# Kernel optimization log

Measured on AMD Instinct MI355X. Metric: run time of the kernel, lower is better.

The kernel has to match this reference:

```python
import jax, jax.numpy as jnp
import numpy as np

GROUPS = 4  # init kwarg


def setup_inputs() -> dict:
    key = jax.random.key(0)
    k1, k2, k3, k4 = jax.random.split(key, 4)
    B, S, D, H = 4, 4096, 256, 10
    # 0.02 scale on weights keeps unscaled QK^T logits in a sane range
    # (original torch code uses raw randn weights and applies NO 1/sqrt(d)
    # scaling inside group_attention, which saturates softmax).
    return {
        "x": jax.random.normal(k1, (B, S, D), dtype=jnp.float32),
        "Wq": jax.random.normal(k2, (H, D, D), dtype=jnp.float32) * 0.02,
        "Wk": jax.random.normal(k3, (H, D, D), dtype=jnp.float32) * 0.02,
        "Wo": jax.random.normal(k4, (D, H * D), dtype=jnp.float32) * 0.02,
    }


def reference(x, Wq, Wk, Wo):
    # x: [B,S,D]; Wq/Wk: [H,D,D]; Wo: [D, H*D] (nn.Linear weight layout)
    H, D, _ = Wq.shape
    B, S, _ = x.shape
    G = GROUPS
    C = S // G  # chunk length

    Q = jnp.einsum('bsd,hde->hbse', x, Wq)  # [H,B,S,D]
    K = jnp.einsum('bsd,hde->hbse', x, Wk)
    # Faithful to source bug: V is projected with wk weights -> V == K

    Qg = Q.reshape(H, B, G, C, D)
    KVg = jnp.roll(K.reshape(H, B, G, C, D), shift=-1, axis=2)  # chunk i attends chunk (i+1)%G

    # NOTE: original applies NO scaling to logits (scale arg unused)
    S_ = jnp.einsum('hbgqd,hbgkd->hbgqk', Qg, KVg)   # [H,B,G,C,C]
    P = jax.nn.softmax(S_, axis=-1)
    O = jnp.einsum('hbgqk,hbgkd->hbgqd', P, KVg)     # [H,B,G,C,D]

    # concat heads on feature dim: [B,S,H*D]
    out = O.reshape(H, B, S, D).transpose(1, 2, 0, 3).reshape(B, S, H * D)
    return jnp.einsum('bsk,dk->bsd', out, Wo)  # final Linear (no bias)
```

## Files before the change

kernel.cpp:

```cpp
#include <hip/hip_runtime.h>

typedef float f32x4 __attribute__((ext_vector_type(4)));
typedef float f32x16 __attribute__((ext_vector_type(16)));
typedef short s16x8 __attribute__((ext_vector_type(8)));
typedef unsigned int u32;

#define BSZ 4
#define SEQ 4096
#define DIM 256
#define NH 10
#define NG 4
#define CHK 1024
#define BS_TOT 16384
#define HD 2560
#define LOG2E 1.44269504f

__device__ __forceinline__ unsigned short f2bf(float f) {
    unsigned int u = __builtin_bit_cast(unsigned int, f);
    u = (u + 0x7fffu + ((u >> 16) & 1u)) >> 16;
    return (unsigned short)u;
}

__device__ __forceinline__ void gload_lds16(const unsigned short* g, unsigned short* l) {
    __builtin_amdgcn_global_load_lds((const __attribute__((address_space(1))) u32*)g,
                                     (__attribute__((address_space(3))) u32*)l, 16, 0, 0);
}

__device__ __forceinline__ u32 cvtpk_bf16(float lo, float hi) {
    u32 r;
    asm("v_cvt_pk_bf16_f32 %0, %1, %2" : "=v"(r) : "v"(lo), "v"(hi));
    return r;
}



__global__ __launch_bounds__(256) void cast_f32_bf16(const float* __restrict__ s,
                                                     unsigned short* __restrict__ d, int n) {
    long i = 4L * (blockIdx.x * 256 + threadIdx.x);
    if (i < n) {
        float4 v = *(const float4*)(s + i);
        ushort4 o;
        o.x = f2bf(v.x); o.y = f2bf(v.y); o.z = f2bf(v.z); o.w = f2bf(v.w);
        *(ushort4*)(d + i) = o;
    }
}

__global__ __launch_bounds__(256) void transpose_cast_w(const float* __restrict__ Wq,
                                                        const float* __restrict__ Wk,
                                                        unsigned short* __restrict__ wqt,
                                                        unsigned short* __restrict__ wkt) {
    const float* W = (blockIdx.z & 1) ? Wk : Wq;
    unsigned short* Wt = (blockIdx.z & 1) ? wkt : wqt;
    int h = blockIdx.z >> 1;
    __shared__ float tile[32][33];
    int d0 = blockIdx.x * 32, e0 = blockIdx.y * 32;
    int tx = threadIdx.x & 31, ty = threadIdx.x >> 5;
    const float* Wh = W + (long)h * 65536;
    unsigned short* Wth = Wt + (long)h * 65536;
#pragma unroll
    for (int r = ty; r < 32; r += 8) tile[r][tx] = Wh[(long)(d0 + r) * 256 + e0 + tx];
    __syncthreads();
#pragma unroll
    for (int r = ty; r < 32; r += 8) Wth[(long)(e0 + r) * 256 + d0 + tx] = f2bf(tile[tx][r]);
}


__device__ __forceinline__ void gemm_body(const unsigned short* __restrict__ A, long lda,
                                          const unsigned short* __restrict__ Bt, long ldb,
                                          unsigned short* Cb, float* Cf, long ldc,
                                          int K, bool accum, long mbase,
                                          unsigned short* KQo, unsigned short* KTo,
                                          float cscale) {
    __shared__ unsigned short As[64 * 40];
    __shared__ unsigned short Bs[256 * 40];
    const int t = threadIdx.x;
    const int w = t >> 6, l = t & 63, lr = l & 15, lg = l >> 4;

    f32x4 acc[16];
#pragma unroll
    for (int i = 0; i < 16; i++) acc[i] = (f32x4){0.f, 0.f, 0.f, 0.f};

    const int ar = t >> 2, akc = (t & 3) * 8;

    for (int k0 = 0; k0 < K; k0 += 32) {
        *(s16x8*)(&As[ar * 40 + akc]) = *(const s16x8*)(A + (mbase + ar) * lda + k0 + akc);
#pragma unroll
        for (int s = 0; s < 4; s++) {
            int n = s * 64 + (t >> 2);
            *(s16x8*)(&Bs[n * 40 + akc]) = *(const s16x8*)(Bt + (long)n * ldb + k0 + akc);
        }
        __syncthreads();
        s16x8 af = *(const s16x8*)(&As[(w * 16 + lr) * 40 + lg * 8]);
        __builtin_amdgcn_s_setprio(1);
#pragma unroll
        for (int nt = 0; nt < 16; nt++) {
            s16x8 bf = *(const s16x8*)(&Bs[(nt * 16 + lr) * 40 + lg * 8]);
            acc[nt] = __builtin_amdgcn_mfma_f32_16x16x32_bf16(af, bf, acc[nt], 0, 0, 0);
        }
        __builtin_amdgcn_s_setprio(0);
        __syncthreads();
    }
    long m0 = mbase + w * 16 + lg * 4;
    if (Cb || Cf) {
#pragma unroll
        for (int nt = 0; nt < 16; nt++) {
            int col = nt * 16 + lr;
#pragma unroll
            for (int r = 0; r < 4; r++) {
                long idx = (m0 + r) * ldc + col;
                if (Cb) {
                    Cb[idx] = f2bf(acc[nt][r] * cscale);
                } else {
                    float v = acc[nt][r];
                    if (accum) v += Cf[idx];
                    Cf[idx] = v;
                }
            }
        }
    }
    if (KQo) {
        int bg = (int)(m0 >> 10);
        int kin = (int)(m0 & 1023);
        int kt = kin >> 5, kw = kin & 31;
        unsigned short* tb = KQo + (long)bg * (256 * 1024) + (long)kt * 8192;
#pragma unroll
        for (int nt = 0; nt < 16; nt++) {
            int d = nt * 16 + lr;
            unsigned short* p = tb + (d >> 4) * 512 + ((d >> 3) & 1) * 256 + (d & 7);
#pragma unroll
            for (int r = 0; r < 4; r++) p[(kw + r) * 8] = f2bf(acc[nt][r]);
        }
    }
    if (KTo) {
        int bg = (int)(m0 >> 10);
        int key0 = (int)(m0 & 1023);
        int kt = key0 >> 5, kw = key0 & 31;
        unsigned short* base = KTo + (long)bg * (256 * 1024) + (long)kt * 8192
                             + (kw >> 4) * 512 + ((kw >> 3) & 1) * 256 + (kw & 7);
#pragma unroll
        for (int nt = 0; nt < 16; nt++) {
            int col = nt * 16 + lr;
            ushort4 v;
            v.x = f2bf(acc[nt][0]); v.y = f2bf(acc[nt][1]);
            v.z = f2bf(acc[nt][2]); v.w = f2bf(acc[nt][3]);
            *(ushort4*)(base + (col >> 5) * 1024 + (col & 31) * 8) = v;
        }
    }
}

__global__ __launch_bounds__(256) void proj_kernel(const unsigned short* __restrict__ xb,
                                                   const unsigned short* __restrict__ wqt,
                                                   const unsigned short* __restrict__ wkt,
                                                   unsigned short* Qb, unsigned short* KQb,
                                                   unsigned short* KTb,
                                                   int h0, long headStrideOut, long headStrideKT) {
    int h = h0 + blockIdx.y;
    bool isK = (blockIdx.z != 0);
    const unsigned short* Bt = (isK ? wkt : wqt) + (long)h * 65536;
    unsigned short* C = isK ? nullptr : (Qb + (long)blockIdx.y * headStrideOut);
    unsigned short* KQo = isK ? (KQb + (long)blockIdx.y * headStrideKT) : nullptr;
    unsigned short* KTo = isK ? (KTb + (long)blockIdx.y * headStrideKT) : nullptr;
    gemm_body(xb, 256, Bt, 256, C, nullptr, 256, 256, false, (long)blockIdx.x * 64,
              KQo, KTo, isK ? 1.0f : LOG2E);
}

__global__ __launch_bounds__(256) void final_kernel(const unsigned short* __restrict__ Ob, long lda,
                                                    const unsigned short* __restrict__ wob, long ldb,
                                                    float* out, int K, int accum) {
    gemm_body(Ob, lda, wob, ldb, nullptr, out, 256, K, accum != 0, (long)blockIdx.x * 64,
              nullptr, nullptr, 1.0f);
}


__global__ __launch_bounds__(256, 3) void proj128(const unsigned short* __restrict__ xb,
                                                  const unsigned short* __restrict__ wqt,
                                                  const unsigned short* __restrict__ wkt,
                                                  unsigned short* __restrict__ Qb,
                                                  unsigned short* __restrict__ KQb,
                                                  unsigned short* __restrict__ KTb,
                                                  long headStrideOut, long headStrideKT) {
    __shared__ unsigned short As[2][128 * 32];
    __shared__ unsigned short Bs[2][128 * 32];

    const int lb = blockIdx.x;
    const int logical = (lb & 7) * 640 + (lb >> 3);
    const int x = logical / 40;
    const int u = logical - x * 40;
    const int mat = u >> 1, ntile = u & 1;
    const int h = mat >> 1;
    const bool isK = (mat & 1) != 0;

    const unsigned short* A = xb;
    const unsigned short* Bt = (isK ? wkt : wqt) + (long)h * 65536 + (long)ntile * 128 * 256;
    const long mbase = (long)x * 128;
    const int ncol0 = ntile * 128;

    const int t = threadIdx.x, w = t >> 6, l = t & 63, lr = l & 15, lg = l >> 4;
    const int wm = w >> 1, wn = w & 1;

    int sOff[2];
#pragma unroll
    for (int i = 0; i < 2; i++) {
        int row = w * 32 + i * 16 + (l >> 2);
        int cs2 = (l & 3) ^ (row & 3);
        sOff[i] = row * 256 + cs2 * 8;
    }

    f32x4 acc[4][4];
#pragma unroll
    for (int i = 0; i < 4; i++)
#pragma unroll
        for (int j = 0; j < 4; j++) acc[i][j] = (f32x4){0.f, 0.f, 0.f, 0.f};

#define PSTAGE(buf, k0) do {                                                     \
        _Pragma("unroll")                                                        \
        for (int i = 0; i < 2; i++)                                              \
            gload_lds16(A + mbase * 256 + (k0) + sOff[i],                        \
                        &As[buf][(w * 32 + i * 16) * 32]);                       \
        _Pragma("unroll")                                                        \
        for (int i = 0; i < 2; i++)                                              \
            gload_lds16(Bt + (k0) + sOff[i],                                     \
                        &Bs[buf][(w * 32 + i * 16) * 32]);                       \
    } while (0)

    PSTAGE(0, 0);
    __syncthreads();
    int cur = 0;
    for (int ks = 0; ks < 8; ++ks) {
        if (ks < 7) PSTAGE(cur ^ 1, (ks + 1) * 32);
        s16x8 a[4], b[4];
#pragma unroll
        for (int mf = 0; mf < 4; mf++) {
            int row = wm * 64 + mf * 16 + lr;
            a[mf] = *(const s16x8*)(&As[cur][row * 32 + (lg ^ (row & 3)) * 8]);
        }
#pragma unroll
        for (int nf = 0; nf < 4; nf++) {
            int row = wn * 64 + nf * 16 + lr;
            b[nf] = *(const s16x8*)(&Bs[cur][row * 32 + (lg ^ (row & 3)) * 8]);
        }
        __builtin_amdgcn_s_setprio(1);
#pragma unroll
        for (int mf = 0; mf < 4; mf++)
#pragma unroll
            for (int nf = 0; nf < 4; nf++)
                acc[mf][nf] = __builtin_amdgcn_mfma_f32_16x16x32_bf16(a[mf], b[nf], acc[mf][nf], 0, 0, 0);
        __builtin_amdgcn_s_setprio(0);
        __syncthreads();
        cur ^= 1;
    }
#undef PSTAGE

    long m0 = mbase + wm * 64 + lg * 4;
    if (!isK) {
        unsigned short* C = Qb + (long)h * headStrideOut;
#pragma unroll
        for (int mf = 0; mf < 4; mf++) {
            long mrow = m0 + mf * 16;
#pragma unroll
            for (int nf = 0; nf < 4; nf++) {
                int col = ncol0 + wn * 64 + nf * 16 + lr;
#pragma unroll
                for (int r = 0; r < 4; r++)
                    C[(mrow + r) * 256 + col] = f2bf(acc[mf][nf][r] * LOG2E);
            }
        }
    } else {
        unsigned short* KQo = KQb + (long)h * headStrideKT;
        unsigned short* KTo = KTb + (long)h * headStrideKT;
#pragma unroll
        for (int mf = 0; mf < 4; mf++) {
            long key = m0 + mf * 16;
            int bg = (int)(key >> 10), kin = (int)(key & 1023);
            int kt = kin >> 5, kw = kin & 31;
            unsigned short* qtb = KQo + (long)bg * (256 * 1024) + (long)kt * 8192;
            unsigned short* vtb = KTo + (long)bg * (256 * 1024) + (long)kt * 8192
                                + (kw >> 4) * 512 + ((kw >> 3) & 1) * 256 + (kw & 7);
#pragma unroll
            for (int nf = 0; nf < 4; nf++) {
                int d = ncol0 + wn * 64 + nf * 16 + lr;
                unsigned short* p = qtb + (d >> 4) * 512 + ((d >> 3) & 1) * 256 + (d & 7);
#pragma unroll
                for (int r = 0; r < 4; r++) p[(kw + r) * 8] = f2bf(acc[mf][nf][r]);
                ushort4 v;
                v.x = f2bf(acc[mf][nf][0]); v.y = f2bf(acc[mf][nf][1]);
                v.z = f2bf(acc[mf][nf][2]); v.w = f2bf(acc[mf][nf][3]);
                *(ushort4*)(vtb + (d >> 5) * 1024 + (d & 31) * 8) = v;
            }
        }
    }
}


__global__ __launch_bounds__(256, 3) void final128(const unsigned short* __restrict__ Ob,
                                                   long headStride,
                                                   const unsigned short* __restrict__ wob,
                                                   float* __restrict__ out) {
    __shared__ unsigned short As[2][128 * 32];
    __shared__ unsigned short Bs[2][128 * 32];

    const int lb = blockIdx.x;
    const int logical = (lb & 7) * 32 + (lb >> 3);
    const int x = logical >> 1, ntile = logical & 1;
    const long mbase = (long)x * 128;
    const int ncol0 = ntile * 128;
    const unsigned short* Bt = wob + (long)ncol0 * HD;

    const int t = threadIdx.x, w = t >> 6, l = t & 63, lr = l & 15, lg = l >> 4;
    const int wm = w >> 1, wn = w & 1;

    int sOffA[2], sOffB[2];
#pragma unroll
    for (int i = 0; i < 2; i++) {
        int row = w * 32 + i * 16 + (l >> 2);
        int cs2 = (l & 3) ^ (row & 3);
        sOffA[i] = row * 256 + cs2 * 8;
        sOffB[i] = row * HD + cs2 * 8;
    }

    f32x4 acc[4][4];
#pragma unroll
    for (int i = 0; i < 4; i++)
#pragma unroll
        for (int j = 0; j < 4; j++) acc[i][j] = (f32x4){0.f, 0.f, 0.f, 0.f};

#define FSTAGE(buf, k0) do {                                                     \
        const unsigned short* Asrc = Ob + (long)((k0) >> 8) * headStride         \
                                   + mbase * 256 + ((k0) & 255);                 \
        _Pragma("unroll")                                                        \
        for (int i = 0; i < 2; i++)                                              \
            gload_lds16(Asrc + sOffA[i], &As[buf][(w * 32 + i * 16) * 32]);      \
        _Pragma("unroll")                                                        \
        for (int i = 0; i < 2; i++)                                              \
            gload_lds16(Bt + (k0) + sOffB[i], &Bs[buf][(w * 32 + i * 16) * 32]); \
    } while (0)

    FSTAGE(0, 0);
    __syncthreads();
    int cur = 0;
    for (int ks = 0; ks < 80; ++ks) {
        if (ks < 79) FSTAGE(cur ^ 1, (ks + 1) * 32);
        s16x8 a[4], b[4];
#pragma unroll
        for (int mf = 0; mf < 4; mf++) {
            int row = wm * 64 + mf * 16 + lr;
            a[mf] = *(const s16x8*)(&As[cur][row * 32 + (lg ^ (row & 3)) * 8]);
        }
#pragma unroll
        for (int nf = 0; nf < 4; nf++) {
            int row = wn * 64 + nf * 16 + lr;
            b[nf] = *(const s16x8*)(&Bs[cur][row * 32 + (lg ^ (row & 3)) * 8]);
        }
        __builtin_amdgcn_s_setprio(1);
#pragma unroll
        for (int mf = 0; mf < 4; mf++)
#pragma unroll
            for (int nf = 0; nf < 4; nf++)
                acc[mf][nf] = __builtin_amdgcn_mfma_f32_16x16x32_bf16(a[mf], b[nf], acc[mf][nf], 0, 0, 0);
        __builtin_amdgcn_s_setprio(0);
        __syncthreads();
        cur ^= 1;
    }
#undef FSTAGE

    long m0 = mbase + wm * 64 + lg * 4;
#pragma unroll
    for (int mf = 0; mf < 4; mf++) {
        long mrow = m0 + mf * 16;
#pragma unroll
        for (int nf = 0; nf < 4; nf++) {
            int col = ncol0 + wn * 64 + nf * 16 + lr;
#pragma unroll
            for (int r = 0; r < 4; r++) out[(mrow + r) * 256 + col] = acc[mf][nf][r];
        }
    }
}


__global__ __launch_bounds__(256, 2) void attn_kernel(const unsigned short* __restrict__ Qb,
                                                      const unsigned short* __restrict__ KQg,
                                                      long headStrideQK,
                                                      const unsigned short* __restrict__ KTg,
                                                      long headStrideKT,
                                                      unsigned short* __restrict__ Ob,
                                                      long ldo, long colStride,
                                                      int chunkPerXcd) {
    const int lb = blockIdx.x;
    const int logical = (lb & 7) * chunkPerXcd + (lb >> 3);
    const int bx = logical & 7;
    const int by = (logical >> 3) & 15;
    const int h = logical >> 7;

    const unsigned short* Q = Qb + (long)h * colStride;
    const unsigned short* KQ = KQg + (long)h * headStrideQK;
    const unsigned short* KT = KTg + (long)h * headStrideKT;
    unsigned short* O = Ob + (long)h * colStride;
    const int b = by >> 2, g = by & 3;
    const long qrow0 = (long)b * SEQ + (long)g * CHK + (long)bx * 128;
    const int bgk = b * NG + ((g + 1) & 3);
    const unsigned short* KQc = KQ + (long)bgk * (256 * 1024);
    const unsigned short* KTc = KT + (long)bgk * (256 * 1024);

    __shared__ unsigned short Klds[2][8192];
    __shared__ unsigned short Vlds[2][8192];

    const int t = threadIdx.x;
    const int w = t >> 6, l = t & 63, l31 = l & 31, hi = l >> 5;

    s16x8 qf[16];
    {
        const unsigned short* qp = Q + (qrow0 + w * 32 + l31) * 256 + hi * 8;
#pragma unroll
        for (int s = 0; s < 16; s++) qf[s] = *(const s16x8*)(qp + s * 16);
    }

    f32x16 o[8];
#pragma unroll
    for (int i = 0; i < 8; i++)
#pragma unroll
        for (int j = 0; j < 16; j++) o[i][j] = 0.f;
    float l_part = 0.f;

#define STAGE(buf, kt_) do {                                                    \
        const unsigned short* Ks = KQc + (long)(kt_) * 8192 + l * 8;            \
        const unsigned short* Vs = KTc + (long)(kt_) * 8192 + l * 8;            \
        _Pragma("unroll")                                                       \
        for (int i = 0; i < 4; i++) {                                           \
            int c = w * 4 + i;                                                  \
            gload_lds16(Ks + c * 512, &Klds[buf][c * 512]);                     \
            gload_lds16(Vs + c * 512, &Vlds[buf][c * 512]);                     \
        }                                                                       \
    } while (0)

    STAGE(0, 0);
    __syncthreads();
    int cur = 0;

    for (int kt = 0; kt < 32; ++kt) {
        if (kt < 31) STAGE(cur ^ 1, kt + 1);

        f32x16 st;
#pragma unroll
        for (int j = 0; j < 16; j++) st[j] = 0.f;
        __builtin_amdgcn_s_setprio(1);
#pragma unroll
        for (int ks = 0; ks < 16; ks++) {
            s16x8 kf = *(const s16x8*)(&Klds[cur][ks * 512 + l * 8]);
            st = __builtin_amdgcn_mfma_f32_32x32x16_bf16(kf, qf[ks], st, 0, 0, 0);
        }
        __builtin_amdgcn_s_setprio(0);

        u32 c0, c1, c2, c3, c4, c5, c6, c7;
        {
            float pa0 = __builtin_amdgcn_exp2f(st[0]),  pa1 = __builtin_amdgcn_exp2f(st[1]);
            float pa2 = __builtin_amdgcn_exp2f(st[2]),  pa3 = __builtin_amdgcn_exp2f(st[3]);
            float pa4 = __builtin_amdgcn_exp2f(st[4]),  pa5 = __builtin_amdgcn_exp2f(st[5]);
            float pa6 = __builtin_amdgcn_exp2f(st[6]),  pa7 = __builtin_amdgcn_exp2f(st[7]);
            float pa8 = __builtin_amdgcn_exp2f(st[8]),  pa9 = __builtin_amdgcn_exp2f(st[9]);
            float paA = __builtin_amdgcn_exp2f(st[10]), paB = __builtin_amdgcn_exp2f(st[11]);
            float paC = __builtin_amdgcn_exp2f(st[12]), paD = __builtin_amdgcn_exp2f(st[13]);
            float paE = __builtin_amdgcn_exp2f(st[14]), paF = __builtin_amdgcn_exp2f(st[15]);
            l_part += (((pa0 + pa1) + (pa2 + pa3)) + ((pa4 + pa5) + (pa6 + pa7)))
                    + (((pa8 + pa9) + (paA + paB)) + ((paC + paD) + (paE + paF)));
            c0 = cvtpk_bf16(pa0, pa1); c1 = cvtpk_bf16(pa2, pa3);
            c2 = cvtpk_bf16(pa4, pa5); c3 = cvtpk_bf16(pa6, pa7);
            c4 = cvtpk_bf16(pa8, pa9); c5 = cvtpk_bf16(paA, paB);
            c6 = cvtpk_bf16(paC, paD); c7 = cvtpk_bf16(paE, paF);
        }
        asm("v_permlane32_swap_b32 %0, %1" : "+v"(c0), "+v"(c2));
        asm("v_permlane32_swap_b32 %0, %1" : "+v"(c1), "+v"(c3));
        asm("v_permlane32_swap_b32 %0, %1" : "+v"(c4), "+v"(c6));
        asm("v_permlane32_swap_b32 %0, %1" : "+v"(c5), "+v"(c7));
        struct { u32 a, b, c, d; } x0 = {c0, c1, c2, c3};
        struct { u32 a, b, c, d; } x1 = {c4, c5, c6, c7};
        s16x8 pa0f = __builtin_bit_cast(s16x8, x0);
        s16x8 pa1f = __builtin_bit_cast(s16x8, x1);

        __builtin_amdgcn_s_setprio(1);
#pragma unroll
        for (int ks = 0; ks < 2; ks++) {
            s16x8 paf = ks ? pa1f : pa0f;
#pragma unroll
            for (int nt = 0; nt < 8; nt++) {
                s16x8 bv = *(const s16x8*)(&Vlds[cur][(nt * 2 + ks) * 512 + l * 8]);
                o[nt] = __builtin_amdgcn_mfma_f32_32x32x16_bf16(paf, bv, o[nt], 0, 0, 0);
            }
        }
        __builtin_amdgcn_s_setprio(0);

        __syncthreads();
        cur ^= 1;
    }
#undef STAGE

    float lt = l_part + __shfl_xor(l_part, 32);
    float rinv = 1.0f / lt;
    float ri[16];
#pragma unroll
    for (int reg = 0; reg < 16; reg++) {
        int qr = (reg & 3) + 8 * (reg >> 2) + 4 * hi;
        ri[reg] = __shfl(rinv, qr);
    }
#pragma unroll
    for (int nt = 0; nt < 8; nt++) {
#pragma unroll
        for (int reg = 0; reg < 16; reg++) {
            int qr = (reg & 3) + 8 * (reg >> 2) + 4 * hi;
            O[(qrow0 + w * 32 + qr) * ldo + nt * 32 + l31] = f2bf(o[nt][reg] * ri[reg]);
        }
    }
}


extern "C" void kernel_launch(void* const* d_in, const int* in_sizes, int n_in,
                              void* d_out, int out_size, void* d_ws, size_t ws_size,
                              hipStream_t stream) {
    const float* x  = (const float*)d_in[0];
    const float* Wq = (const float*)d_in[1];
    const float* Wk = (const float*)d_in[2];
    const float* Wo = (const float*)d_in[3];
    float* out = (float*)d_out;
    char* ws = (char*)d_ws;

    unsigned short* xb  = (unsigned short*)(ws);
    unsigned short* wqt = (unsigned short*)(ws + 8388608);
    unsigned short* wkt = (unsigned short*)(ws + 9699328);
    unsigned short* wob = (unsigned short*)(ws + 11010048);
    char* dyn = ws + 12320768;

    cast_f32_bf16<<<4096, 256, 0, stream>>>(x, xb, BS_TOT * DIM);
    cast_f32_bf16<<<640, 256, 0, stream>>>(Wo, wob, DIM * HD);
    transpose_cast_w<<<dim3(8, 8, 2 * NH), 256, 0, stream>>>(Wq, Wk, wqt, wkt);

    const long perHeadElems = (long)BS_TOT * DIM;
    const size_t FULL_NEED = 12320768ULL + 3ULL * 83886080ULL;

    if (ws_size >= FULL_NEED) {
        unsigned short* Qb  = (unsigned short*)dyn;
        unsigned short* KQb = Qb + (long)NH * perHeadElems;
        unsigned short* KTb = KQb + (long)NH * perHeadElems;
        proj128<<<5120, 256, 0, stream>>>(xb, wqt, wkt, Qb, KQb, KTb,
                                          perHeadElems, perHeadElems);
        attn_kernel<<<1280, 256, 0, stream>>>(Qb, KQb, perHeadElems, KTb, perHeadElems,
                                              Qb, 256, perHeadElems, 160);
        final128<<<256, 256, 0, stream>>>(Qb, perHeadElems, wob, out);
    } else {
        unsigned short* Qh  = (unsigned short*)dyn;
        unsigned short* KQh = Qh + perHeadElems;
        unsigned short* KTh = KQh + perHeadElems;
        hipMemsetAsync(d_out, 0, (size_t)out_size * 4, stream);
        for (int h = 0; h < NH; ++h) {
            proj_kernel<<<dim3(256, 1, 2), 256, 0, stream>>>(xb, wqt, wkt, Qh, KQh, KTh, h, 0, 0);
            attn_kernel<<<128, 256, 0, stream>>>(Qh, KQh, 0, KTh, 0, Qh, 256, 0, 16);
            final_kernel<<<256, 256, 0, stream>>>(Qh, 256, wob + h * 256, HD, out, 256, 1);
        }
    }
}
```

Baseline: 344.0 us.

## Software-pipeline PV MFMAs one tile behind QK to overlap softmax

Restructures the attention inner loop so the P·V matmul for the previous key tile is interleaved with the QK^T MFMAs for the current tile, with a drain step after the loop. K and V staging are split so that V for tile kt is loaded during iteration kt and consumed in kt+1. The aim is to hide exp and pack latency and keep the matrix units busy. The cost is extra live registers for the previous P fragments and a more complex buffer schedule, which may reduce occupancy.

```diff
diff --git a/kernel.cpp b/kernel.cpp
--- a/kernel.cpp
+++ b/kernel.cpp
@@ -421,32 +421,53 @@
         for (int j = 0; j < 16; j++) o[i][j] = 0.f;
     float l_part = 0.f;
 
-#define STAGE(buf, kt_) do {                                                    \
+#define STAGE_K(buf, kt_) do {                                                  \
         const unsigned short* Ks = KQc + (long)(kt_) * 8192 + l * 8;            \
+        _Pragma("unroll")                                                       \
+        for (int i = 0; i < 4; i++) {                                           \
+            int c = w * 4 + i;                                                  \
+            gload_lds16(Ks + c * 512, &Klds[buf][c * 512]);                     \
+        }                                                                       \
+    } while (0)
+#define STAGE_V(buf, kt_) do {                                                  \
         const unsigned short* Vs = KTc + (long)(kt_) * 8192 + l * 8;            \
         _Pragma("unroll")                                                       \
         for (int i = 0; i < 4; i++) {                                           \
             int c = w * 4 + i;                                                  \
-            gload_lds16(Ks + c * 512, &Klds[buf][c * 512]);                     \
             gload_lds16(Vs + c * 512, &Vlds[buf][c * 512]);                     \
         }                                                                       \
     } while (0)
 
-    STAGE(0, 0);
+    STAGE_K(0, 0);
     __syncthreads();
-    int cur = 0;
+
+    s16x8 paPrev0 = {}, paPrev1 = {};
 
     for (int kt = 0; kt < 32; ++kt) {
-        if (kt < 31) STAGE(cur ^ 1, kt + 1);
+        const int cur = kt & 1;
+        if (kt < 31) STAGE_K(cur ^ 1, kt + 1);
+        STAGE_V(cur, kt);
 
         f32x16 st;
 #pragma unroll
         for (int j = 0; j < 16; j++) st[j] = 0.f;
         __builtin_amdgcn_s_setprio(1);
-#pragma unroll
-        for (int ks = 0; ks < 16; ks++) {
-            s16x8 kf = *(const s16x8*)(&Klds[cur][ks * 512 + l * 8]);
-            st = __builtin_amdgcn_mfma_f32_32x32x16_bf16(kf, qf[ks], st, 0, 0, 0);
+        if (kt > 0) {
+#pragma unroll
+            for (int ks = 0; ks < 16; ks++) {
+                s16x8 kf = *(const s16x8*)(&Klds[cur][ks * 512 + l * 8]);
+                st = __builtin_amdgcn_mfma_f32_32x32x16_bf16(kf, qf[ks], st, 0, 0, 0);
+                int nt = ks & 7, ks2 = ks >> 3;
+                s16x8 bv = *(const s16x8*)(&Vlds[cur ^ 1][(nt * 2 + ks2) * 512 + l * 8]);
+                o[nt] = __builtin_amdgcn_mfma_f32_32x32x16_bf16(ks2 ? paPrev1 : paPrev0,
+                                                                bv, o[nt], 0, 0, 0);
+            }
+        } else {
+#pragma unroll
+            for (int ks = 0; ks < 16; ks++) {
+                s16x8 kf = *(const s16x8*)(&Klds[cur][ks * 512 + l * 8]);
+                st = __builtin_amdgcn_mfma_f32_32x32x16_bf16(kf, qf[ks], st, 0, 0, 0);
+            }
         }
         __builtin_amdgcn_s_setprio(0);
 
@@ -473,25 +494,23 @@
         asm("v_permlane32_swap_b32 %0, %1" : "+v"(c5), "+v"(c7));
         struct { u32 a, b, c, d; } x0 = {c0, c1, c2, c3};
         struct { u32 a, b, c, d; } x1 = {c4, c5, c6, c7};
-        s16x8 pa0f = __builtin_bit_cast(s16x8, x0);
-        s16x8 pa1f = __builtin_bit_cast(s16x8, x1);
-
-        __builtin_amdgcn_s_setprio(1);
-#pragma unroll
-        for (int ks = 0; ks < 2; ks++) {
-            s16x8 paf = ks ? pa1f : pa0f;
-#pragma unroll
-            for (int nt = 0; nt < 8; nt++) {
-                s16x8 bv = *(const s16x8*)(&Vlds[cur][(nt * 2 + ks) * 512 + l * 8]);
-                o[nt] = __builtin_amdgcn_mfma_f32_32x32x16_bf16(paf, bv, o[nt], 0, 0, 0);
-            }
-        }
-        __builtin_amdgcn_s_setprio(0);
+        paPrev0 = __builtin_bit_cast(s16x8, x0);
+        paPrev1 = __builtin_bit_cast(s16x8, x1);
 
         __syncthreads();
-        cur ^= 1;
-    }
-#undef STAGE
+    }
+#undef STAGE_K
+#undef STAGE_V
+
+    __builtin_amdgcn_s_setprio(1);
+#pragma unroll
+    for (int ks = 0; ks < 16; ks++) {
+        int nt = ks & 7, ks2 = ks >> 3;
+        s16x8 bv = *(const s16x8*)(&Vlds[1][(nt * 2 + ks2) * 512 + l * 8]);
+        o[nt] = __builtin_amdgcn_mfma_f32_32x32x16_bf16(ks2 ? paPrev1 : paPrev0,
+                                                        bv, o[nt], 0, 0, 0);
+    }
+    __builtin_amdgcn_s_setprio(0);
 
     float lt = l_part + __shfl_xor(l_part, 32);
     float rinv = 1.0f / lt;
```

Result: slower. 352.5 us (+2.5%).

## Process two 32-row query tiles per wave in attention to reuse K/V fragments

Applied to the files above, without the earlier changes.

Each wave now handles 64 query rows (two 32-row tiles) instead of 32, so every K and V fragment read from LDS feeds two MFMAs. The block count halves and occupancy is lowered to one block per CU to make room for the doubled accumulator and Q registers. This is meant to cut LDS read traffic and the global K/V staging done per query row. The cost is much higher register pressure, fewer resident waves and less parallelism for hiding latency, and possible spilling.

```diff
diff --git a/kernel.cpp b/kernel.cpp
--- a/kernel.cpp
+++ b/kernel.cpp
@@ -32,6 +32,32 @@
     return r;
 }
 
+
+__device__ __forceinline__ void softmax_pack(const f32x16& st, float& l_part,
+                                             s16x8& p0, s16x8& p1) {
+    float e0 = __builtin_amdgcn_exp2f(st[0]),  e1 = __builtin_amdgcn_exp2f(st[1]);
+    float e2 = __builtin_amdgcn_exp2f(st[2]),  e3 = __builtin_amdgcn_exp2f(st[3]);
+    float e4 = __builtin_amdgcn_exp2f(st[4]),  e5 = __builtin_amdgcn_exp2f(st[5]);
+    float e6 = __builtin_amdgcn_exp2f(st[6]),  e7 = __builtin_amdgcn_exp2f(st[7]);
+    float e8 = __builtin_amdgcn_exp2f(st[8]),  e9 = __builtin_amdgcn_exp2f(st[9]);
+    float eA = __builtin_amdgcn_exp2f(st[10]), eB = __builtin_amdgcn_exp2f(st[11]);
+    float eC = __builtin_amdgcn_exp2f(st[12]), eD = __builtin_amdgcn_exp2f(st[13]);
+    float eE = __builtin_amdgcn_exp2f(st[14]), eF = __builtin_amdgcn_exp2f(st[15]);
+    l_part += (((e0 + e1) + (e2 + e3)) + ((e4 + e5) + (e6 + e7)))
+            + (((e8 + e9) + (eA + eB)) + ((eC + eD) + (eE + eF)));
+    u32 c0 = cvtpk_bf16(e0, e1), c1 = cvtpk_bf16(e2, e3);
+    u32 c2 = cvtpk_bf16(e4, e5), c3 = cvtpk_bf16(e6, e7);
+    u32 c4 = cvtpk_bf16(e8, e9), c5 = cvtpk_bf16(eA, eB);
+    u32 c6 = cvtpk_bf16(eC, eD), c7 = cvtpk_bf16(eE, eF);
+    asm("v_permlane32_swap_b32 %0, %1" : "+v"(c0), "+v"(c2));
+    asm("v_permlane32_swap_b32 %0, %1" : "+v"(c1), "+v"(c3));
+    asm("v_permlane32_swap_b32 %0, %1" : "+v"(c4), "+v"(c6));
+    asm("v_permlane32_swap_b32 %0, %1" : "+v"(c5), "+v"(c7));
+    struct { u32 a, b, c, d; } x0 = {c0, c1, c2, c3};
+    struct { u32 a, b, c, d; } x1 = {c4, c5, c6, c7};
+    p0 = __builtin_bit_cast(s16x8, x0);
+    p1 = __builtin_bit_cast(s16x8, x1);
+}
 
 
 __global__ __launch_bounds__(256) void cast_f32_bf16(const float* __restrict__ s,
@@ -377,7 +403,7 @@
 }
 
 
-__global__ __launch_bounds__(256, 2) void attn_kernel(const unsigned short* __restrict__ Qb,
+__global__ __launch_bounds__(256, 1) void attn_kernel(const unsigned short* __restrict__ Qb,
                                                       const unsigned short* __restrict__ KQg,
                                                       long headStrideQK,
                                                       const unsigned short* __restrict__ KTg,
@@ -387,16 +413,16 @@
                                                       int chunkPerXcd) {
     const int lb = blockIdx.x;
     const int logical = (lb & 7) * chunkPerXcd + (lb >> 3);
-    const int bx = logical & 7;
-    const int by = (logical >> 3) & 15;
-    const int h = logical >> 7;
+    const int bx = logical & 3;
+    const int by = (logical >> 2) & 15;
+    const int h = logical >> 6;
 
     const unsigned short* Q = Qb + (long)h * colStride;
     const unsigned short* KQ = KQg + (long)h * headStrideQK;
     const unsigned short* KT = KTg + (long)h * headStrideKT;
     unsigned short* O = Ob + (long)h * colStride;
     const int b = by >> 2, g = by & 3;
-    const long qrow0 = (long)b * SEQ + (long)g * CHK + (long)bx * 128;
+    const long qrow0 = (long)b * SEQ + (long)g * CHK + (long)bx * 256;
     const int bgk = b * NG + ((g + 1) & 3);
     const unsigned short* KQc = KQ + (long)bgk * (256 * 1024);
     const unsigned short* KTc = KT + (long)bgk * (256 * 1024);
@@ -407,19 +433,23 @@
     const int t = threadIdx.x;
     const int w = t >> 6, l = t & 63, l31 = l & 31, hi = l >> 5;
 
-    s16x8 qf[16];
+    s16x8 qfA[16], qfB[16];
     {
-        const unsigned short* qp = Q + (qrow0 + w * 32 + l31) * 256 + hi * 8;
-#pragma unroll
-        for (int s = 0; s < 16; s++) qf[s] = *(const s16x8*)(qp + s * 16);
-    }
-
-    f32x16 o[8];
+        const unsigned short* qpA = Q + (qrow0 + w * 64 + l31) * 256 + hi * 8;
+        const unsigned short* qpB = qpA + 32 * 256;
+#pragma unroll
+        for (int s = 0; s < 16; s++) {
+            qfA[s] = *(const s16x8*)(qpA + s * 16);
+            qfB[s] = *(const s16x8*)(qpB + s * 16);
+        }
+    }
+
+    f32x16 oA[8], oB[8];
 #pragma unroll
     for (int i = 0; i < 8; i++)
 #pragma unroll
-        for (int j = 0; j < 16; j++) o[i][j] = 0.f;
-    float l_part = 0.f;
+        for (int j = 0; j < 16; j++) { oA[i][j] = 0.f; oB[i][j] = 0.f; }
+    float lpA = 0.f, lpB = 0.f;
 
 #define STAGE(buf, kt_) do {                                                    \
         const unsigned short* Ks = KQc + (long)(kt_) * 8192 + l * 8;            \
@@ -439,51 +469,32 @@
     for (int kt = 0; kt < 32; ++kt) {
         if (kt < 31) STAGE(cur ^ 1, kt + 1);
 
-        f32x16 st;
-#pragma unroll
-        for (int j = 0; j < 16; j++) st[j] = 0.f;
+        f32x16 stA, stB;
+#pragma unroll
+        for (int j = 0; j < 16; j++) { stA[j] = 0.f; stB[j] = 0.f; }
         __builtin_amdgcn_s_setprio(1);
 #pragma unroll
         for (int ks = 0; ks < 16; ks++) {
             s16x8 kf = *(const s16x8*)(&Klds[cur][ks * 512 + l * 8]);
-            st = __builtin_amdgcn_mfma_f32_32x32x16_bf16(kf, qf[ks], st, 0, 0, 0);
+            stA = __builtin_amdgcn_mfma_f32_32x32x16_bf16(kf, qfA[ks], stA, 0, 0, 0);
+            stB = __builtin_amdgcn_mfma_f32_32x32x16_bf16(kf, qfB[ks], stB, 0, 0, 0);
         }
         __builtin_amdgcn_s_setprio(0);
 
-        u32 c0, c1, c2, c3, c4, c5, c6, c7;
-        {
-            float pa0 = __builtin_amdgcn_exp2f(st[0]),  pa1 = __builtin_amdgcn_exp2f(st[1]);
-            float pa2 = __builtin_amdgcn_exp2f(st[2]),  pa3 = __builtin_amdgcn_exp2f(st[3]);
-            float pa4 = __builtin_amdgcn_exp2f(st[4]),  pa5 = __builtin_amdgcn_exp2f(st[5]);
-            float pa6 = __builtin_amdgcn_exp2f(st[6]),  pa7 = __builtin_amdgcn_exp2f(st[7]);
-            float pa8 = __builtin_amdgcn_exp2f(st[8]),  pa9 = __builtin_amdgcn_exp2f(st[9]);
-            float paA = __builtin_amdgcn_exp2f(st[10]), paB = __builtin_amdgcn_exp2f(st[11]);
-            float paC = __builtin_amdgcn_exp2f(st[12]), paD = __builtin_amdgcn_exp2f(st[13]);
-            float paE = __builtin_amdgcn_exp2f(st[14]), paF = __builtin_amdgcn_exp2f(st[15]);
-            l_part += (((pa0 + pa1) + (pa2 + pa3)) + ((pa4 + pa5) + (pa6 + pa7)))
-                    + (((pa8 + pa9) + (paA + paB)) + ((paC + paD) + (paE + paF)));
-            c0 = cvtpk_bf16(pa0, pa1); c1 = cvtpk_bf16(pa2, pa3);
-            c2 = cvtpk_bf16(pa4, pa5); c3 = cvtpk_bf16(pa6, pa7);
-            c4 = cvtpk_bf16(pa8, pa9); c5 = cvtpk_bf16(paA, paB);
-            c6 = cvtpk_bf16(paC, paD); c7 = cvtpk_bf16(paE, paF);
-        }
-        asm("v_permlane32_swap_b32 %0, %1" : "+v"(c0), "+v"(c2));
-        asm("v_permlane32_swap_b32 %0, %1" : "+v"(c1), "+v"(c3));
-        asm("v_permlane32_swap_b32 %0, %1" : "+v"(c4), "+v"(c6));
-        asm("v_permlane32_swap_b32 %0, %1" : "+v"(c5), "+v"(c7));
-        struct { u32 a, b, c, d; } x0 = {c0, c1, c2, c3};
-        struct { u32 a, b, c, d; } x1 = {c4, c5, c6, c7};
-        s16x8 pa0f = __builtin_bit_cast(s16x8, x0);
-        s16x8 pa1f = __builtin_bit_cast(s16x8, x1);
+        s16x8 paA0, paA1, paB0, paB1;
+        softmax_pack(stA, lpA, paA0, paA1);
+        softmax_pack(stB, lpB, paB0, paB1);
 
         __builtin_amdgcn_s_setprio(1);
 #pragma unroll
         for (int ks = 0; ks < 2; ks++) {
-            s16x8 paf = ks ? pa1f : pa0f;
+            s16x8 pA = ks ? paA1 : paA0;
+            s16x8 pB = ks ? paB1 : paB0;
 #pragma unroll
             for (int nt = 0; nt < 8; nt++) {
                 s16x8 bv = *(const s16x8*)(&Vlds[cur][(nt * 2 + ks) * 512 + l * 8]);
-                o[nt] = __builtin_amdgcn_mfma_f32_32x32x16_bf16(paf, bv, o[nt], 0, 0, 0);
+                oA[nt] = __builtin_amdgcn_mfma_f32_32x32x16_bf16(pA, bv, oA[nt], 0, 0, 0);
+                oB[nt] = __builtin_amdgcn_mfma_f32_32x32x16_bf16(pB, bv, oB[nt], 0, 0, 0);
             }
         }
         __builtin_amdgcn_s_setprio(0);
@@ -493,20 +504,26 @@
     }
 #undef STAGE
 
-    float lt = l_part + __shfl_xor(l_part, 32);
-    float rinv = 1.0f / lt;
-    float ri[16];
-#pragma unroll
-    for (int reg = 0; reg < 16; reg++) {
-        int qr = (reg & 3) + 8 * (reg >> 2) + 4 * hi;
-        ri[reg] = __shfl(rinv, qr);
-    }
-#pragma unroll
-    for (int nt = 0; nt < 8; nt++) {
+#pragma unroll
+    for (int half = 0; half < 2; half++) {
+        float lp = half ? lpB : lpA;
+        float lt = lp + __shfl_xor(lp, 32);
+        float rinv = 1.0f / lt;
+        float ri[16];
 #pragma unroll
         for (int reg = 0; reg < 16; reg++) {
             int qr = (reg & 3) + 8 * (reg >> 2) + 4 * hi;
-            O[(qrow0 + w * 32 + qr) * ldo + nt * 32 + l31] = f2bf(o[nt][reg] * ri[reg]);
+            ri[reg] = __shfl(rinv, qr);
+        }
+        long orow0 = qrow0 + w * 64 + half * 32;
+#pragma unroll
+        for (int nt = 0; nt < 8; nt++) {
+#pragma unroll
+            for (int reg = 0; reg < 16; reg++) {
+                int qr = (reg & 3) + 8 * (reg >> 2) + 4 * hi;
+                float v = half ? oB[nt][reg] : oA[nt][reg];
+                O[(orow0 + qr) * ldo + nt * 32 + l31] = f2bf(v * ri[reg]);
+            }
         }
     }
 }
@@ -541,8 +558,8 @@
         unsigned short* KTb = KQb + (long)NH * perHeadElems;
         proj128<<<5120, 256, 0, stream>>>(xb, wqt, wkt, Qb, KQb, KTb,
                                           perHeadElems, perHeadElems);
-        attn_kernel<<<1280, 256, 0, stream>>>(Qb, KQb, perHeadElems, KTb, perHeadElems,
-                                              Qb, 256, perHeadElems, 160);
+        attn_kernel<<<640, 256, 0, stream>>>(Qb, KQb, perHeadElems, KTb, perHeadElems,
+                                             Qb, 256, perHeadElems, 80);
         final128<<<256, 256, 0, stream>>>(Qb, perHeadElems, wob, out);
     } else {
         unsigned short* Qh  = (unsigned short*)dyn;
@@ -551,7 +568,7 @@
         hipMemsetAsync(d_out, 0, (size_t)out_size * 4, stream);
         for (int h = 0; h < NH; ++h) {
             proj_kernel<<<dim3(256, 1, 2), 256, 0, stream>>>(xb, wqt, wkt, Qh, KQh, KTh, h, 0, 0);
-            attn_kernel<<<128, 256, 0, stream>>>(Qh, KQh, 0, KTh, 0, Qh, 256, 0, 16);
+            attn_kernel<<<64, 256, 0, stream>>>(Qh, KQh, 0, KTh, 0, Qh, 256, 0, 8);
             final_kernel<<<256, 256, 0, stream>>>(Qh, 256, wob + h * 256, HD, out, 256, 1);
         }
     }
```

Result: slower. 388.6 us (+13.0%).
